# Performance work log

Hardware: AMD Instinct MI355X
Metric: run time of the kernel (lower is better)

## Reference

```python
import jax, jax.numpy as jnp
import numpy as np

N_NODES = 100000
N_EDGES = 100000
NNZ = 1600000
C_IN = 128
C_OUT = 128


def setup_inputs() -> dict:
    key = jax.random.key(0)
    k1, k2, k3, k4, k5 = jax.random.split(key, 5)
    x_0 = jax.random.normal(k1, (N_NODES, C_IN), dtype=jnp.float32)
    node_idx = jax.random.randint(k2, (NNZ,), 0, N_NODES, dtype=jnp.int64)
    edge_idx = jnp.sort(jax.random.randint(k3, (NNZ,), 0, N_EDGES, dtype=jnp.int64))
    values = jnp.ones((NNZ,), dtype=jnp.float32)
    weight = jax.random.normal(k4, (C_IN, C_OUT), dtype=jnp.float32) * (1.0 / np.sqrt(C_IN))
    att_weight = jax.random.normal(k5, (2 * C_IN, 1), dtype=jnp.float32) * 0.1
    return {"x_0": x_0, "node_idx": node_idx, "edge_idx": edge_idx,
            "values": values, "weight": weight, "att_weight": att_weight}


def reference(x_0, node_idx, edge_idx, values, weight, att_weight):
    # Step 1: m_0_1 = B1^T @ x_0  -> hyperedge features [n_edges, C_in]
    m_0_1 = jax.ops.segment_sum(values[:, None] * x_0[node_idx], edge_idx,
                                num_segments=N_EDGES)
    # Attention per nonzero (node i, hyperedge j):
    # elu(cat(m_0_1[j], x_0[i]) @ att_weight)  == elu((m01@a_src)[j] + (x0@a_tgt)[i])
    a_src = att_weight[:C_IN, 0]
    a_tgt = att_weight[C_IN:, 0]
    scores = jax.nn.elu((m_0_1 @ a_src)[edge_idx] + (x_0 @ a_tgt)[node_idx])  # [nnz]
    # x_message = m_0_1 @ Theta
    x_message = m_0_1 @ weight  # [n_edges, C_out]
    # Attention-weighted scatter back to nodes: (B1 * att) @ x_message
    out = jax.ops.segment_sum((scores * values)[:, None] * x_message[edge_idx],
                              node_idx, num_segments=N_NODES)
    return out
```

## Files before the change

kernel.cpp:

```cpp
#include <hip/hip_runtime.h>
#include <math.h>

#define N_NODES 100000
#define N_EDGES 100000
#define NNZT    1600000
#define C       128
#define NB      ((N_NODES + 255) >> 8)
#define CHUNK   4096
#define ORDCAP  6144

typedef _Float16 half8 __attribute__((ext_vector_type(8)));
typedef _Float16 h2    __attribute__((ext_vector_type(2)));
typedef float    f32x4 __attribute__((ext_vector_type(4)));

__global__ __launch_bounds__(256) void k1_node_dot(
    const float* __restrict__ x0, const float* __restrict__ att,
    float* __restrict__ t_node, _Float16* __restrict__ x0h)
{
    int wave = threadIdx.x >> 6;
    int lane = threadIdx.x & 63;
    int node = blockIdx.x * 4 + wave;
    const float2 xv = *reinterpret_cast<const float2*>(x0 + (size_t)node * C + lane * 2);
    h2 hx = { (_Float16)xv.x, (_Float16)xv.y };
    *reinterpret_cast<h2*>(x0h + (size_t)node * C + lane * 2) = hx;
    const float2 av = *reinterpret_cast<const float2*>(att + C + lane * 2);
    float v = xv.x * av.x + xv.y * av.y;
    #pragma unroll
    for (int off = 32; off > 0; off >>= 1) v += __shfl_xor(v, off, 64);
    if (lane == 0) t_node[node] = v;
}

__global__ __launch_bounds__(256) void k_rowptr(
    const int* __restrict__ edge_idx, int* __restrict__ row_start)
{
    int e = blockIdx.x * 256 + threadIdx.x;
    if (e >= NNZT) return;
    int j = edge_idx[e];
    int jprev = (e == 0) ? -1 : edge_idx[e - 1];
    for (int k = jprev + 1; k <= j; ++k) row_start[k] = e;
    if (e == NNZT - 1)
        for (int k = j + 1; k <= N_EDGES; ++k) row_start[k] = NNZT;
}

__global__ __launch_bounds__(256) void k_wcvt(
    const float* __restrict__ W, _Float16* __restrict__ wt)
{
    int i = blockIdx.x * 256 + threadIdx.x;
    int k = i >> 7, n = i & 127;
    wt[(size_t)n * C + k] = (_Float16)W[(size_t)k * C + n];
}

__global__ __launch_bounds__(256) void k2_edge_msg(
    const half8* __restrict__ x0h,
    const int*   __restrict__ node_idx,
    const int*   __restrict__ row_start,
    const float* __restrict__ values,
    const float* __restrict__ att,
    _Float16* __restrict__ m01h,
    float* __restrict__ s_edge)
{
    int wave = threadIdx.x >> 6;
    int lane = threadIdx.x & 63;
    int j    = blockIdx.x * 4 + wave;
    int sub  = lane >> 4;
    int ln   = lane & 15;
    int start = row_start[j];
    int end   = row_start[j + 1];

    h2 hacc[4];
    #pragma unroll
    for (int q = 0; q < 4; ++q) hacc[q] = (h2){(_Float16)0.f, (_Float16)0.f};

    int e = start + sub;
    for (; e + 4 < end; e += 8) {
        int   n0 = node_idx[e];
        int   n1 = node_idx[e + 4];
        _Float16 v0 = (_Float16)values[e];
        _Float16 v1 = (_Float16)values[e + 4];
        h2 v0p = {v0, v0}, v1p = {v1, v1};
        half8 A = x0h[(size_t)n0 * 16 + ln];
        half8 B = x0h[(size_t)n1 * 16 + ln];
        const h2* a2 = reinterpret_cast<const h2*>(&A);
        const h2* b2 = reinterpret_cast<const h2*>(&B);
        #pragma unroll
        for (int q = 0; q < 4; ++q)
            hacc[q] = a2[q] * v0p + (b2[q] * v1p + hacc[q]);
    }
    if (e < end) {
        int   n0 = node_idx[e];
        _Float16 v0 = (_Float16)values[e];
        h2 v0p = {v0, v0};
        half8 A = x0h[(size_t)n0 * 16 + ln];
        const h2* a2 = reinterpret_cast<const h2*>(&A);
        #pragma unroll
        for (int q = 0; q < 4; ++q) hacc[q] = a2[q] * v0p + hacc[q];
    }

    float f[8];
    #pragma unroll
    for (int q = 0; q < 4; ++q) {
        f[2 * q]     = (float)hacc[q][0];
        f[2 * q + 1] = (float)hacc[q][1];
    }
    #pragma unroll
    for (int q = 0; q < 8; ++q) {
        f[q] += __shfl_xor(f[q], 16, 64);
        f[q] += __shfl_xor(f[q], 32, 64);
    }
    if (lane < 16) {
        half8 hv;
        #pragma unroll
        for (int q = 0; q < 8; ++q) hv[q] = (_Float16)f[q];
        reinterpret_cast<half8*>(m01h + (size_t)j * C)[ln] = hv;
    }
    f32x4 a0 = *reinterpret_cast<const f32x4*>(att + ln * 8);
    f32x4 a1 = *reinterpret_cast<const f32x4*>(att + ln * 8 + 4);
    float p = f[0] * a0[0] + f[1] * a0[1] + f[2] * a0[2] + f[3] * a0[3]
            + f[4] * a1[0] + f[5] * a1[1] + f[6] * a1[2] + f[7] * a1[3];
    #pragma unroll
    for (int off = 8; off > 0; off >>= 1) p += __shfl_xor(p, off, 64);
    if (lane == 0) s_edge[j] = p;
}

__global__ __launch_bounds__(256) void k_bhist(
    const int* __restrict__ node_idx, int* __restrict__ btot)
{
    __shared__ int cnt4[4][NB];
    int tid = threadIdx.x;
    int w   = tid >> 6;
    for (int b = tid; b < 4 * NB; b += 256) (&cnt4[0][0])[b] = 0;
    __syncthreads();
    const int per = (NNZT + 255) / 256;
    int e0 = blockIdx.x * per;
    int e1 = e0 + per; if (e1 > NNZT) e1 = NNZT;
    for (int e = e0 + tid; e < e1; e += 256)
        atomicAdd(&cnt4[w][node_idx[e] >> 8], 1);
    __syncthreads();
    for (int b = tid; b < NB; b += 256) {
        int cc = cnt4[0][b] + cnt4[1][b] + cnt4[2][b] + cnt4[3][b];
        if (cc) atomicAdd(&btot[b], cc);
    }
}

__global__ __launch_bounds__(512) void k_bscan(
    const int* __restrict__ btot, int* __restrict__ bbase, int* __restrict__ bcur)
{
    __shared__ int s[512];
    int tid = threadIdx.x;
    int v = (tid < NB) ? btot[tid] : 0;
    s[tid] = v;
    __syncthreads();
    for (int off = 1; off < 512; off <<= 1) {
        int t = (tid >= off) ? s[tid - off] : 0;
        __syncthreads();
        s[tid] += t;
        __syncthreads();
    }
    if (tid < NB) { bbase[tid] = s[tid] - v; bcur[tid] = s[tid] - v; }
    if (tid == NB - 1) bbase[NB] = s[tid];
}

__global__ __launch_bounds__(512) void k_part(
    const int*   __restrict__ node_idx,
    const int*   __restrict__ edge_idx,
    const float* __restrict__ values,
    const float* __restrict__ s_edge,
    const float* __restrict__ t_node,
    int*  __restrict__ bcur,
    int2* __restrict__ rec)
{
    __shared__ int hist[NB];
    __shared__ int lbase[NB];
    __shared__ int gb[NB];
    __shared__ int cur[NB];
    __shared__ int2 lrec[CHUNK];
    __shared__ unsigned short lbid[CHUNK];
    int tid = threadIdx.x;
    int e0 = blockIdx.x * CHUNK;
    int m = NNZT - e0; if (m > CHUNK) m = CHUNK;

    for (int b = tid; b < NB; b += 512) hist[b] = 0;
    __syncthreads();
    for (int i = tid; i < m; i += 512)
        atomicAdd(&hist[node_idx[e0 + i] >> 8], 1);
    __syncthreads();
    int c = (tid < NB) ? hist[tid] : 0;
    for (int off = 1; off < NB; off <<= 1) {
        int t = 0;
        if (tid < NB && tid >= off) t = hist[tid - off];
        __syncthreads();
        if (tid < NB) hist[tid] += t;
        __syncthreads();
    }
    if (tid < NB) {
        int excl = hist[tid] - c;
        lbase[tid] = excl;
        cur[tid]   = excl;
        gb[tid]    = c ? atomicAdd(&bcur[tid], c) : 0;
    }
    __syncthreads();
    for (int i = tid; i < m; i += 512) {
        int e = e0 + i;
        int n = node_idx[e];
        int b = n >> 8;
        int j = edge_idx[e];
        float v = values[e];
        float s = s_edge[j] + t_node[n];
        float coef = (s > 0.f ? s : expm1f(s)) * v;
        int slot = atomicAdd(&cur[b], 1);
        lrec[slot] = make_int2(((n & 255) << 17) | j, __float_as_int(coef));
        lbid[slot] = (unsigned short)b;
    }
    __syncthreads();
    for (int s = tid; s < m; s += 512) {
        int b = lbid[s];
        rec[gb[b] + (s - lbase[b])] = lrec[s];
    }
}

__global__ __launch_bounds__(512) void k_bgather(
    const int2*  __restrict__ rec,
    const int*   __restrict__ bbase,
    const half8* __restrict__ m01h,
    _Float16* __restrict__ yh)
{
    __shared__ int cnt[256];
    __shared__ int bl[256];
    __shared__ int cur[256];
    __shared__ unsigned short ord[ORDCAP];
    int b = blockIdx.x, tid = threadIdx.x;
    int lo = bbase[b], hi = bbase[b + 1];
    int m = hi - lo;
    int mm = m < ORDCAP ? m : ORDCAP;

    if (tid < 256) cnt[tid] = 0;
    __syncthreads();
    for (int i = tid; i < mm; i += 512)
        atomicAdd(&cnt[((unsigned)rec[lo + i].x) >> 17], 1);
    __syncthreads();
    if (tid < 256) bl[tid] = cnt[tid];
    __syncthreads();
    for (int off = 1; off < 256; off <<= 1) {
        int t = 0;
        if (tid < 256 && tid >= off) t = bl[tid - off];
        __syncthreads();
        if (tid < 256) bl[tid] += t;
        __syncthreads();
    }
    if (tid < 256) cur[tid] = bl[tid] - cnt[tid];
    __syncthreads();
    for (int i = tid; i < mm; i += 512) {
        int local = ((unsigned)rec[lo + i].x) >> 17;
        int p = atomicAdd(&cur[local], 1);
        ord[p] = (unsigned short)i;
    }
    __syncthreads();

    int wave = tid >> 6, lane = tid & 63, sub = lane >> 4, ln = lane & 15;
    for (int local = wave; local < 256; local += 8) {
        int n = (b << 8) + local;
        if (n >= N_NODES) break;
        int cb = bl[local] - cnt[local];
        int cc = cnt[local];
        float facc[8];
        #pragma unroll
        for (int q = 0; q < 8; ++q) facc[q] = 0.f;
        int i = sub;
        for (; i + 4 < cc; i += 8) {
            int2 r0 = rec[lo + ord[cb + i]];
            int2 r1 = rec[lo + ord[cb + i + 4]];
            half8 a0 = m01h[(size_t)(r0.x & 0x1FFFF) * 16 + ln];
            half8 a1 = m01h[(size_t)(r1.x & 0x1FFFF) * 16 + ln];
            float c0 = __int_as_float(r0.y);
            float c1 = __int_as_float(r1.y);
            #pragma unroll
            for (int q = 0; q < 8; ++q)
                facc[q] += c0 * (float)a0[q] + c1 * (float)a1[q];
        }
        if (i < cc) {
            int2 r0 = rec[lo + ord[cb + i]];
            half8 a0 = m01h[(size_t)(r0.x & 0x1FFFF) * 16 + ln];
            float c0 = __int_as_float(r0.y);
            #pragma unroll
            for (int q = 0; q < 8; ++q) facc[q] += c0 * (float)a0[q];
        }
        for (int x = ORDCAP + sub; x < m; x += 4) {
            int2 r = rec[lo + x];
            if ((int)(((unsigned)r.x) >> 17) == local) {
                float c0 = __int_as_float(r.y);
                half8 a0 = m01h[(size_t)(r.x & 0x1FFFF) * 16 + ln];
                #pragma unroll
                for (int q = 0; q < 8; ++q) facc[q] += c0 * (float)a0[q];
            }
        }
        #pragma unroll
        for (int q = 0; q < 8; ++q) {
            facc[q] += __shfl_xor(facc[q], 16, 64);
            facc[q] += __shfl_xor(facc[q], 32, 64);
        }
        if (lane < 16) {
            half8 hv;
            #pragma unroll
            for (int q = 0; q < 8; ++q) hv[q] = (_Float16)facc[q];
            reinterpret_cast<half8*>(yh + (size_t)n * C)[ln] = hv;
        }
    }
}

__global__ __launch_bounds__(64) void k4_mfma(
    const _Float16* __restrict__ yh,
    const _Float16* __restrict__ wt,
    float* __restrict__ out)
{
    int lane = threadIdx.x;
    int m    = lane & 15;
    int quad = lane >> 4;
    int rb   = blockIdx.x * 16;
    const _Float16* yrow = yh + (size_t)(rb + m) * C + quad * 8;
    half8 a[4];
    #pragma unroll
    for (int kc = 0; kc < 4; ++kc)
        a[kc] = *reinterpret_cast<const half8*>(yrow + kc * 32);
    #pragma unroll
    for (int ct = 0; ct < 8; ++ct) {
        const _Float16* wrow = wt + (size_t)(ct * 16 + m) * C + quad * 8;
        f32x4 acc = {0.f, 0.f, 0.f, 0.f};
        #pragma unroll
        for (int kc = 0; kc < 4; ++kc) {
            half8 b = *reinterpret_cast<const half8*>(wrow + kc * 32);
            acc = __builtin_amdgcn_mfma_f32_16x16x32_f16(a[kc], b, acc, 0, 0, 0);
        }
        int orow = rb + quad * 4;
        int ocol = ct * 16 + m;
        #pragma unroll
        for (int r = 0; r < 4; ++r)
            out[(size_t)(orow + r) * C + ocol] = acc[r];
    }
}

extern "C" void kernel_launch(void* const* d_in, const int* in_sizes, int n_in,
                              void* d_out, int out_size, void* d_ws, size_t ws_size,
                              hipStream_t stream)
{
    const float* x0       = (const float*)d_in[0];
    const int*   node_idx = (const int*)  d_in[1];
    const int*   edge_idx = (const int*)  d_in[2];
    const float* values   = (const float*)d_in[3];
    const float* W        = (const float*)d_in[4];
    const float* att      = (const float*)d_in[5];
    float* out = (float*)d_out;

    _Float16* x0h_s  = (_Float16*)d_out;
    _Float16* m01h_s = x0h_s + (size_t)N_NODES * C;
    int2* rec = (int2*)d_out;

    char*  p   = (char*)d_ws;
    _Float16* yh    = (_Float16*)p; p += (size_t)N_NODES * C * sizeof(_Float16);
    float* t_node   = (float*)p;  p += N_NODES * sizeof(float);
    float* s_edge   = (float*)p;  p += N_EDGES * sizeof(float);
    int*   btot     = (int*)p;    p += 512 * sizeof(int);
    int*   bbase    = (int*)p;    p += 512 * sizeof(int);
    int*   bcur     = (int*)p;    p += 512 * sizeof(int);
    int*   row_start= (int*)p;    p += (N_EDGES + 1) * sizeof(int);
    _Float16* wt    = (_Float16*)p; p += (size_t)C * C * sizeof(_Float16);

    hipMemsetAsync(btot, 0, NB * sizeof(int), stream);

    k1_node_dot<<<N_NODES / 4, 256, 0, stream>>>(x0, att, t_node, x0h_s);
    k_rowptr<<<(NNZT + 255) / 256, 256, 0, stream>>>(edge_idx, row_start);
    k_wcvt  <<<(C * C + 255) / 256, 256, 0, stream>>>(W, wt);
    k2_edge_msg<<<N_EDGES / 4, 256, 0, stream>>>((const half8*)x0h_s, node_idx, row_start,
                                                 values, att, m01h_s, s_edge);

    k_bhist<<<256, 256, 0, stream>>>(node_idx, btot);
    k_bscan<<<1, 512, 0, stream>>>(btot, bbase, bcur);
    k_part <<<(NNZT + CHUNK - 1) / CHUNK, 512, 0, stream>>>(node_idx, edge_idx, values,
                                                            s_edge, t_node, bcur, rec);
    k_bgather<<<NB, 512, 0, stream>>>(rec, bbase, (const half8*)m01h_s, yh);
    k4_mfma<<<N_NODES / 16, 64, 0, stream>>>(yh, wt, out);
}
```

Baseline: 358.3 us.

## Split bucket gather across four blocks with LDS-staged records and deeper unroll

The per-bucket gather kernel is split so that four 256-thread blocks each handle 64 of the bucket's 256 nodes. This raises the block count from about 391 to about 1564, which gives better occupancy. Each block copies its matching records into shared memory instead of an index array, so the inner loop no longer does an indirect global load per record. If a quarter holds more than 2048 records, a slow fallback scans the whole bucket. Both the gather loops and the edge-message kernel are unrolled to four outstanding row loads to raise memory-level parallelism, at the cost of every block re-reading the bucket's record list twice.

```diff
diff --git a/kernel.cpp b/kernel.cpp
--- a/kernel.cpp
+++ b/kernel.cpp
@@ -7,7 +7,8 @@
 #define C       128
 #define NB      ((N_NODES + 255) >> 8)
 #define CHUNK   4096
-#define ORDCAP  6144
+#define SPLIT   4
+#define LCAP    2048
 
 typedef _Float16 half8 __attribute__((ext_vector_type(8)));
 typedef _Float16 h2    __attribute__((ext_vector_type(2)));
@@ -72,9 +73,34 @@
     for (int q = 0; q < 4; ++q) hacc[q] = (h2){(_Float16)0.f, (_Float16)0.f};
 
     int e = start + sub;
+    for (; e + 12 < end; e += 16) {
+        int n0 = node_idx[e];
+        int n1 = node_idx[e + 4];
+        int n2 = node_idx[e + 8];
+        int n3 = node_idx[e + 12];
+        float f0 = values[e];
+        float f1 = values[e + 4];
+        float f2 = values[e + 8];
+        float f3 = values[e + 12];
+        half8 A  = x0h[(size_t)n0 * 16 + ln];
+        half8 B  = x0h[(size_t)n1 * 16 + ln];
+        half8 Cg = x0h[(size_t)n2 * 16 + ln];
+        half8 D  = x0h[(size_t)n3 * 16 + ln];
+        _Float16 v0 = (_Float16)f0, v1 = (_Float16)f1;
+        _Float16 v2 = (_Float16)f2, v3 = (_Float16)f3;
+        h2 v0p = {v0, v0}, v1p = {v1, v1}, v2p = {v2, v2}, v3p = {v3, v3};
+        const h2* a2 = reinterpret_cast<const h2*>(&A);
+        const h2* b2 = reinterpret_cast<const h2*>(&B);
+        const h2* c2 = reinterpret_cast<const h2*>(&Cg);
+        const h2* d2 = reinterpret_cast<const h2*>(&D);
+        #pragma unroll
+        for (int q = 0; q < 4; ++q)
+            hacc[q] = a2[q] * v0p
+                    + (b2[q] * v1p + (c2[q] * v2p + (d2[q] * v3p + hacc[q])));
+    }
     for (; e + 4 < end; e += 8) {
-        int   n0 = node_idx[e];
-        int   n1 = node_idx[e + 4];
+        int n0 = node_idx[e];
+        int n1 = node_idx[e + 4];
         _Float16 v0 = (_Float16)values[e];
         _Float16 v1 = (_Float16)values[e + 4];
         h2 v0p = {v0, v0}, v1p = {v1, v1};
@@ -87,7 +113,7 @@
             hacc[q] = a2[q] * v0p + (b2[q] * v1p + hacc[q]);
     }
     if (e < end) {
-        int   n0 = node_idx[e];
+        int n0 = node_idx[e];
         _Float16 v0 = (_Float16)values[e];
         h2 v0p = {v0, v0};
         half8 A = x0h[(size_t)n0 * 16 + ln];
@@ -218,79 +244,111 @@
     }
 }
 
-__global__ __launch_bounds__(512) void k_bgather(
+__global__ __launch_bounds__(256) void k_bgather(
     const int2*  __restrict__ rec,
     const int*   __restrict__ bbase,
     const half8* __restrict__ m01h,
     _Float16* __restrict__ yh)
 {
-    __shared__ int cnt[256];
-    __shared__ int bl[256];
-    __shared__ int cur[256];
-    __shared__ unsigned short ord[ORDCAP];
-    int b = blockIdx.x, tid = threadIdx.x;
+    __shared__ int cnt[64], bl[64], cur[64];
+    __shared__ int2 lrec[LCAP];
+    __shared__ int ovf;
+    int bid  = blockIdx.x;
+    int b    = bid >> 2;
+    int part = bid & 3;
+    int tid  = threadIdx.x;
     int lo = bbase[b], hi = bbase[b + 1];
-    int m = hi - lo;
-    int mm = m < ORDCAP ? m : ORDCAP;
-
-    if (tid < 256) cnt[tid] = 0;
-    __syncthreads();
-    for (int i = tid; i < mm; i += 512)
-        atomicAdd(&cnt[((unsigned)rec[lo + i].x) >> 17], 1);
-    __syncthreads();
-    if (tid < 256) bl[tid] = cnt[tid];
-    __syncthreads();
-    for (int off = 1; off < 256; off <<= 1) {
+    int m  = hi - lo;
+    int l0 = part << 6;
+
+    if (tid < 64) cnt[tid] = 0;
+    if (tid == 0) ovf = 0;
+    __syncthreads();
+    for (int i = tid; i < m; i += 256) {
+        int d = (int)(((unsigned)rec[lo + i].x) >> 17) - l0;
+        if ((unsigned)d < 64u) atomicAdd(&cnt[d], 1);
+    }
+    __syncthreads();
+    if (tid < 64) bl[tid] = cnt[tid];
+    __syncthreads();
+    for (int off = 1; off < 64; off <<= 1) {
         int t = 0;
-        if (tid < 256 && tid >= off) t = bl[tid - off];
-        __syncthreads();
-        if (tid < 256) bl[tid] += t;
-        __syncthreads();
-    }
-    if (tid < 256) cur[tid] = bl[tid] - cnt[tid];
-    __syncthreads();
-    for (int i = tid; i < mm; i += 512) {
-        int local = ((unsigned)rec[lo + i].x) >> 17;
-        int p = atomicAdd(&cur[local], 1);
-        ord[p] = (unsigned short)i;
+        if (tid < 64 && tid >= off) t = bl[tid - off];
+        __syncthreads();
+        if (tid < 64) bl[tid] += t;
+        __syncthreads();
+    }
+    if (tid < 64) cur[tid] = bl[tid] - cnt[tid];
+    if (tid == 63 && bl[63] > LCAP) ovf = 1;
+    __syncthreads();
+    if (!ovf) {
+        for (int i = tid; i < m; i += 256) {
+            int2 r = rec[lo + i];
+            int d = (int)(((unsigned)r.x) >> 17) - l0;
+            if ((unsigned)d < 64u) {
+                int p = atomicAdd(&cur[d], 1);
+                lrec[p] = r;
+            }
+        }
     }
     __syncthreads();
 
     int wave = tid >> 6, lane = tid & 63, sub = lane >> 4, ln = lane & 15;
-    for (int local = wave; local < 256; local += 8) {
-        int n = (b << 8) + local;
+    for (int d = wave; d < 64; d += 4) {
+        int n = (b << 8) + l0 + d;
         if (n >= N_NODES) break;
-        int cb = bl[local] - cnt[local];
-        int cc = cnt[local];
+        int cb = bl[d] - cnt[d];
+        int cc = cnt[d];
         float facc[8];
         #pragma unroll
         for (int q = 0; q < 8; ++q) facc[q] = 0.f;
-        int i = sub;
-        for (; i + 4 < cc; i += 8) {
-            int2 r0 = rec[lo + ord[cb + i]];
-            int2 r1 = rec[lo + ord[cb + i + 4]];
-            half8 a0 = m01h[(size_t)(r0.x & 0x1FFFF) * 16 + ln];
-            half8 a1 = m01h[(size_t)(r1.x & 0x1FFFF) * 16 + ln];
-            float c0 = __int_as_float(r0.y);
-            float c1 = __int_as_float(r1.y);
-            #pragma unroll
-            for (int q = 0; q < 8; ++q)
-                facc[q] += c0 * (float)a0[q] + c1 * (float)a1[q];
-        }
-        if (i < cc) {
-            int2 r0 = rec[lo + ord[cb + i]];
-            half8 a0 = m01h[(size_t)(r0.x & 0x1FFFF) * 16 + ln];
-            float c0 = __int_as_float(r0.y);
-            #pragma unroll
-            for (int q = 0; q < 8; ++q) facc[q] += c0 * (float)a0[q];
-        }
-        for (int x = ORDCAP + sub; x < m; x += 4) {
-            int2 r = rec[lo + x];
-            if ((int)(((unsigned)r.x) >> 17) == local) {
-                float c0 = __int_as_float(r.y);
-                half8 a0 = m01h[(size_t)(r.x & 0x1FFFF) * 16 + ln];
+        if (!ovf) {
+            int i = sub;
+            for (; i + 12 < cc; i += 16) {
+                int2 r0 = lrec[cb + i];
+                int2 r1 = lrec[cb + i + 4];
+                int2 r2 = lrec[cb + i + 8];
+                int2 r3 = lrec[cb + i + 12];
+                half8 a0 = m01h[(size_t)(r0.x & 0x1FFFF) * 16 + ln];
+                half8 a1 = m01h[(size_t)(r1.x & 0x1FFFF) * 16 + ln];
+                half8 a2 = m01h[(size_t)(r2.x & 0x1FFFF) * 16 + ln];
+                half8 a3 = m01h[(size_t)(r3.x & 0x1FFFF) * 16 + ln];
+                float c0 = __int_as_float(r0.y);
+                float c1 = __int_as_float(r1.y);
+                float c2 = __int_as_float(r2.y);
+                float c3 = __int_as_float(r3.y);
+                #pragma unroll
+                for (int q = 0; q < 8; ++q)
+                    facc[q] += c0 * (float)a0[q] + c1 * (float)a1[q]
+                             + c2 * (float)a2[q] + c3 * (float)a3[q];
+            }
+            for (; i + 4 < cc; i += 8) {
+                int2 r0 = lrec[cb + i];
+                int2 r1 = lrec[cb + i + 4];
+                half8 a0 = m01h[(size_t)(r0.x & 0x1FFFF) * 16 + ln];
+                half8 a1 = m01h[(size_t)(r1.x & 0x1FFFF) * 16 + ln];
+                float c0 = __int_as_float(r0.y);
+                float c1 = __int_as_float(r1.y);
+                #pragma unroll
+                for (int q = 0; q < 8; ++q)
+                    facc[q] += c0 * (float)a0[q] + c1 * (float)a1[q];
+            }
+            if (i < cc) {
+                int2 r0 = lrec[cb + i];
+                half8 a0 = m01h[(size_t)(r0.x & 0x1FFFF) * 16 + ln];
+                float c0 = __int_as_float(r0.y);
                 #pragma unroll
                 for (int q = 0; q < 8; ++q) facc[q] += c0 * (float)a0[q];
+            }
+        } else {
+            for (int x = sub; x < m; x += 4) {
+                int2 r = rec[lo + x];
+                if ((int)(((unsigned)r.x) >> 17) == l0 + d) {
+                    float c0 = __int_as_float(r.y);
+                    half8 a0 = m01h[(size_t)(r.x & 0x1FFFF) * 16 + ln];
+                    #pragma unroll
+                    for (int q = 0; q < 8; ++q) facc[q] += c0 * (float)a0[q];
+                }
             }
         }
         #pragma unroll
@@ -376,6 +434,6 @@
     k_bscan<<<1, 512, 0, stream>>>(btot, bbase, bcur);
     k_part <<<(NNZT + CHUNK - 1) / CHUNK, 512, 0, stream>>>(node_idx, edge_idx, values,
                                                             s_edge, t_node, bcur, rec);
-    k_bgather<<<NB, 512, 0, stream>>>(rec, bbase, (const half8*)m01h_s, yh);
+    k_bgather<<<NB * SPLIT, 256, 0, stream>>>(rec, bbase, (const half8*)m01h_s, yh);
     k4_mfma<<<N_NODES / 16, 64, 0, stream>>>(yh, wt, out);
 }
```

After: 336.2 us. -6.2%, faster.
